# Performance work log

Measured on AMD Instinct MI355X. Metric: run time of the kernel, lower is better.

The kernel has to match this reference:

```python
import jax, jax.numpy as jnp
import numpy as np

B, T, U, D, V = 2, 512, 128, 512, 1024


def setup_inputs() -> dict:
    key = jax.random.key(0)
    k1, k2, k3 = jax.random.split(key, 3)
    encoder_outputs = jax.random.normal(k1, (B, T, D), dtype=jnp.float32)
    decoder_outputs = jax.random.normal(k2, (B, U, D), dtype=jnp.float32)
    # fc = Linear(2*D, V, bias=False): weight shape (V, 2*D)
    W = jax.random.normal(k3, (V, 2 * D), dtype=jnp.float32) * (1.0 / np.sqrt(2 * D))
    return {"encoder_outputs": encoder_outputs, "decoder_outputs": decoder_outputs, "W": W}


def reference(encoder_outputs, decoder_outputs, W):
    # Faithful to: cat(enc.repeat over U, dec.repeat over T, dim=-1) @ W.T
    # Since the Linear has no bias, splitting W into encoder/decoder halves and
    # broadcast-adding the two projections is exactly the same math, without
    # materializing the (B,T,U,2D) concat tensor.
    d = encoder_outputs.shape[-1]
    W_enc = W[:, :d]   # (V, D) acts on encoder half
    W_dec = W[:, d:]   # (V, D) acts on decoder half
    enc_proj = jnp.einsum("btd,vd->btv", encoder_outputs, W_enc)  # (B,T,V)
    dec_proj = jnp.einsum("bud,vd->buv", decoder_outputs, W_dec)  # (B,U,V)
    # (B,T,U,V)
    return enc_proj[:, :, None, :] + dec_proj[:, None, :, :]
```

## Files before the change

### kernel.cpp

```cpp
#include <hip/hip_runtime.h>

#define BB 2
#define TT 512
#define UU 128
#define DD 512
#define VV 1024

typedef float float4v __attribute__((ext_vector_type(4)));
typedef float f32x4   __attribute__((ext_vector_type(4)));
typedef short short8  __attribute__((ext_vector_type(8)));

__device__ __forceinline__ unsigned short f2bf(float f) {
    unsigned u = __builtin_bit_cast(unsigned, f);
    unsigned r = (u + 0x7FFFu + ((u >> 16) & 1u)) >> 16;
    return (unsigned short)r;
}

__device__ __forceinline__ short8 pack_bf16_8(float4v lo, float4v hi) {
    short8 r;
    r[0] = (short)f2bf(lo.x); r[1] = (short)f2bf(lo.y);
    r[2] = (short)f2bf(lo.z); r[3] = (short)f2bf(lo.w);
    r[4] = (short)f2bf(hi.x); r[5] = (short)f2bf(hi.y);
    r[6] = (short)f2bf(hi.z); r[7] = (short)f2bf(hi.w);
    return r;
}

__global__ __launch_bounds__(256) void proj_gemm_mfma(
    const float* __restrict__ Aenc,
    const float* __restrict__ Adec,
    const float* __restrict__ W,
    float* __restrict__ Cenc,
    float* __restrict__ Cdec)
{
    __shared__ alignas(16) unsigned short sA[64][40];
    __shared__ alignas(16) unsigned short sB[64][40];

    const int bid = blockIdx.x;
    const float* A; const float* Wp; float* C;
    int tile_m, tile_n;
    if (bid < 256) {
        A = Aenc; Wp = W;      C = Cenc;
        tile_m = bid >> 4; tile_n = bid & 15;
    } else {
        int b2 = bid - 256;
        A = Adec; Wp = W + DD; C = Cdec;
        tile_m = b2 >> 4; tile_n = b2 & 15;
    }
    const int row0 = tile_m * 64;
    const int col0 = tile_n * 64;

    const int tid  = threadIdx.x;
    const int lane = tid & 63;
    const int wave = tid >> 6;
    const int wr   = wave >> 1;
    const int wc   = wave & 1;
    const int lrow = lane & 15;
    const int kg   = lane >> 4;

    const int srow = tid >> 2;
    const int schk = tid & 3;

    f32x4 acc[2][2] = {};

    for (int k0 = 0; k0 < DD; k0 += 32) {
        const float* ap = &A [(size_t)(row0 + srow) * DD      + k0 + schk * 8];
        const float* wp = &Wp[(size_t)(col0 + srow) * (2*DD)  + k0 + schk * 8];
        float4v a0 = *(const float4v*)ap;
        float4v a1 = *(const float4v*)(ap + 4);
        float4v w0 = *(const float4v*)wp;
        float4v w1 = *(const float4v*)(wp + 4);
        short8 av = pack_bf16_8(a0, a1);
        short8 wv = pack_bf16_8(w0, w1);

        __syncthreads();
        *(short8*)&sA[srow][schk * 8] = av;
        *(short8*)&sB[srow][schk * 8] = wv;
        __syncthreads();

        short8 af0 = *(const short8*)&sA[wr * 32 +      lrow][kg * 8];
        short8 af1 = *(const short8*)&sA[wr * 32 + 16 + lrow][kg * 8];
        short8 bf0 = *(const short8*)&sB[wc * 32 +      lrow][kg * 8];
        short8 bf1 = *(const short8*)&sB[wc * 32 + 16 + lrow][kg * 8];

        acc[0][0] = __builtin_amdgcn_mfma_f32_16x16x32_bf16(af0, bf0, acc[0][0], 0, 0, 0);
        acc[0][1] = __builtin_amdgcn_mfma_f32_16x16x32_bf16(af0, bf1, acc[0][1], 0, 0, 0);
        acc[1][0] = __builtin_amdgcn_mfma_f32_16x16x32_bf16(af1, bf0, acc[1][0], 0, 0, 0);
        acc[1][1] = __builtin_amdgcn_mfma_f32_16x16x32_bf16(af1, bf1, acc[1][1], 0, 0, 0);
    }

    #pragma unroll
    for (int mi = 0; mi < 2; ++mi) {
        #pragma unroll
        for (int ni = 0; ni < 2; ++ni) {
            const int r0 = row0 + wr * 32 + mi * 16 + kg * 4;
            const int c  = col0 + wc * 32 + ni * 16 + lrow;
            #pragma unroll
            for (int j = 0; j < 4; ++j)
                C[(size_t)(r0 + j) * VV + c] = acc[mi][ni][j];
        }
    }
}

__global__ __launch_bounds__(256) void bcast_add_kernel(
    const float* __restrict__ enc_proj,
    const float* __restrict__ dec_proj,
    float* __restrict__ out)
{
    const int blk  = blockIdx.x;
    const int bt   = blk >> 1;
    const int half = blk & 1;
    const int b    = bt >> 9;
    const int tid  = threadIdx.x;
    const int voff = tid * 4;

    float4v e = *(const float4v*)&enc_proj[(size_t)bt * VV + voff];
    const float* dbase = dec_proj + (size_t)b * UU * VV;
    float*       obase = out      + (size_t)bt * UU * VV;

    const int u0 = half * (UU / 2);
    #pragma unroll 4
    for (int u = u0; u < u0 + (UU / 2); ++u) {
        float4v d = *(const float4v*)&dbase[(size_t)u * VV + voff];
        float4v r = e + d;
        __builtin_nontemporal_store(r, (float4v*)&obase[(size_t)u * VV + voff]);
    }
}

extern "C" void kernel_launch(void* const* d_in, const int* in_sizes, int n_in,
                              void* d_out, int out_size, void* d_ws, size_t ws_size,
                              hipStream_t stream) {
    (void)in_sizes; (void)n_in; (void)out_size; (void)ws_size;
    const float* enc = (const float*)d_in[0];
    const float* dec = (const float*)d_in[1];
    const float* W   = (const float*)d_in[2];
    float* out = (float*)d_out;

    float* enc_proj = (float*)d_ws;
    float* dec_proj = enc_proj + (size_t)BB * TT * VV;

    proj_gemm_mfma<<<dim3(320), dim3(256), 0, stream>>>(enc, dec, W, enc_proj, dec_proj);
    bcast_add_kernel<<<dim3(BB * TT * 2), dim3(256), 0, stream>>>(enc_proj, dec_proj, out);
}
```

Before: 540.7 us.

## Fuse encoder projection GEMM with broadcast-add epilogue, separate decoder GEMM

Splits the projection into a small decoder GEMM kernel and an encoder GEMM kernel whose epilogue stages the tile in shared memory and writes all U broadcast sums directly. This removes the enc_proj workspace round trip and the separate broadcast kernel. The trade-off is that the large output write is now done by only 256 blocks, one per CU, with a strided row pattern, which reduces store parallelism.

```diff
diff --git a/kernel.cpp b/kernel.cpp
--- a/kernel.cpp
+++ b/kernel.cpp
@@ -25,29 +25,19 @@
     return r;
 }
 
-__global__ __launch_bounds__(256) void proj_gemm_mfma(
-    const float* __restrict__ Aenc,
+__global__ __launch_bounds__(256) void dec_gemm_mfma(
     const float* __restrict__ Adec,
     const float* __restrict__ W,
-    float* __restrict__ Cenc,
     float* __restrict__ Cdec)
 {
     __shared__ alignas(16) unsigned short sA[64][40];
     __shared__ alignas(16) unsigned short sB[64][40];
 
-    const int bid = blockIdx.x;
-    const float* A; const float* Wp; float* C;
-    int tile_m, tile_n;
-    if (bid < 256) {
-        A = Aenc; Wp = W;      C = Cenc;
-        tile_m = bid >> 4; tile_n = bid & 15;
-    } else {
-        int b2 = bid - 256;
-        A = Adec; Wp = W + DD; C = Cdec;
-        tile_m = b2 >> 4; tile_n = b2 & 15;
-    }
+    const int tile_m = blockIdx.x >> 4;
+    const int tile_n = blockIdx.x & 15;
     const int row0 = tile_m * 64;
     const int col0 = tile_n * 64;
+    const float* Wp = W + DD;
 
     const int tid  = threadIdx.x;
     const int lane = tid & 63;
@@ -56,15 +46,14 @@
     const int wc   = wave & 1;
     const int lrow = lane & 15;
     const int kg   = lane >> 4;
-
     const int srow = tid >> 2;
     const int schk = tid & 3;
 
     f32x4 acc[2][2] = {};
 
     for (int k0 = 0; k0 < DD; k0 += 32) {
-        const float* ap = &A [(size_t)(row0 + srow) * DD      + k0 + schk * 8];
-        const float* wp = &Wp[(size_t)(col0 + srow) * (2*DD)  + k0 + schk * 8];
+        const float* ap = &Adec[(size_t)(row0 + srow) * DD     + k0 + schk * 8];
+        const float* wp = &Wp  [(size_t)(col0 + srow) * (2*DD) + k0 + schk * 8];
         float4v a0 = *(const float4v*)ap;
         float4v a1 = *(const float4v*)(ap + 4);
         float4v w0 = *(const float4v*)wp;
@@ -89,40 +78,99 @@
     }
 
     #pragma unroll
-    for (int mi = 0; mi < 2; ++mi) {
+    for (int mi = 0; mi < 2; ++mi)
         #pragma unroll
         for (int ni = 0; ni < 2; ++ni) {
             const int r0 = row0 + wr * 32 + mi * 16 + kg * 4;
             const int c  = col0 + wc * 32 + ni * 16 + lrow;
             #pragma unroll
             for (int j = 0; j < 4; ++j)
-                C[(size_t)(r0 + j) * VV + c] = acc[mi][ni][j];
+                Cdec[(size_t)(r0 + j) * VV + c] = acc[mi][ni][j];
         }
-    }
 }
 
-__global__ __launch_bounds__(256) void bcast_add_kernel(
-    const float* __restrict__ enc_proj,
+__global__ __launch_bounds__(256) void enc_gemm_bcast(
+    const float* __restrict__ Aenc,
+    const float* __restrict__ W,
     const float* __restrict__ dec_proj,
     float* __restrict__ out)
 {
-    const int blk  = blockIdx.x;
-    const int bt   = blk >> 1;
-    const int half = blk & 1;
-    const int b    = bt >> 9;
+    __shared__ alignas(16) unsigned short sA[64][40];
+    __shared__ alignas(16) unsigned short sB[64][40];
+    __shared__ alignas(16) float sT[64][68];
+
+    const int tile_m = blockIdx.x >> 4;
+    const int tile_n = blockIdx.x & 15;
+    const int row0 = tile_m * 64;
+    const int col0 = tile_n * 64;
+
     const int tid  = threadIdx.x;
-    const int voff = tid * 4;
+    const int lane = tid & 63;
+    const int wave = tid >> 6;
+    const int wr   = wave >> 1;
+    const int wc   = wave & 1;
+    const int lrow = lane & 15;
+    const int kg   = lane >> 4;
+    const int srow = tid >> 2;
+    const int schk = tid & 3;
 
-    float4v e = *(const float4v*)&enc_proj[(size_t)bt * VV + voff];
-    const float* dbase = dec_proj + (size_t)b * UU * VV;
-    float*       obase = out      + (size_t)bt * UU * VV;
+    f32x4 acc[2][2] = {};
 
-    const int u0 = half * (UU / 2);
-    #pragma unroll 4
-    for (int u = u0; u < u0 + (UU / 2); ++u) {
-        float4v d = *(const float4v*)&dbase[(size_t)u * VV + voff];
-        float4v r = e + d;
-        __builtin_nontemporal_store(r, (float4v*)&obase[(size_t)u * VV + voff]);
+    for (int k0 = 0; k0 < DD; k0 += 32) {
+        const float* ap = &Aenc[(size_t)(row0 + srow) * DD     + k0 + schk * 8];
+        const float* wp = &W   [(size_t)(col0 + srow) * (2*DD) + k0 + schk * 8];
+        float4v a0 = *(const float4v*)ap;
+        float4v a1 = *(const float4v*)(ap + 4);
+        float4v w0 = *(const float4v*)wp;
+        float4v w1 = *(const float4v*)(wp + 4);
+        short8 av = pack_bf16_8(a0, a1);
+        short8 wv = pack_bf16_8(w0, w1);
+
+        __syncthreads();
+        *(short8*)&sA[srow][schk * 8] = av;
+        *(short8*)&sB[srow][schk * 8] = wv;
+        __syncthreads();
+
+        short8 af0 = *(const short8*)&sA[wr * 32 +      lrow][kg * 8];
+        short8 af1 = *(const short8*)&sA[wr * 32 + 16 + lrow][kg * 8];
+        short8 bf0 = *(const short8*)&sB[wc * 32 +      lrow][kg * 8];
+        short8 bf1 = *(const short8*)&sB[wc * 32 + 16 + lrow][kg * 8];
+
+        acc[0][0] = __builtin_amdgcn_mfma_f32_16x16x32_bf16(af0, bf0, acc[0][0], 0, 0, 0);
+        acc[0][1] = __builtin_amdgcn_mfma_f32_16x16x32_bf16(af0, bf1, acc[0][1], 0, 0, 0);
+        acc[1][0] = __builtin_amdgcn_mfma_f32_16x16x32_bf16(af1, bf0, acc[1][0], 0, 0, 0);
+        acc[1][1] = __builtin_amdgcn_mfma_f32_16x16x32_bf16(af1, bf1, acc[1][1], 0, 0, 0);
+    }
+
+    #pragma unroll
+    for (int mi = 0; mi < 2; ++mi)
+        #pragma unroll
+        for (int ni = 0; ni < 2; ++ni) {
+            const int r0 = wr * 32 + mi * 16 + kg * 4;
+            const int c  = wc * 32 + ni * 16 + lrow;
+            #pragma unroll
+            for (int j = 0; j < 4; ++j)
+                sT[r0 + j][c] = acc[mi][ni][j];
+        }
+    __syncthreads();
+
+    const int vq = tid & 15;
+    const int pr = tid >> 4;
+    const int b  = row0 >> 9;
+
+    const float* dbase = dec_proj + ((size_t)b * UU) * VV + col0 + vq * 4;
+    float* obase = out + ((size_t)(row0 + pr) * UU) * VV + col0 + vq * 4;
+    const size_t tstep = (size_t)16 * UU * VV;
+
+    #pragma unroll 2
+    for (int u = 0; u < UU; ++u) {
+        float4v d = *(const float4v*)&dbase[(size_t)u * VV];
+        float* op = obase + (size_t)u * VV;
+        #pragma unroll
+        for (int tr = 0; tr < 4; ++tr) {
+            float4v e = *(const float4v*)&sT[tr * 16 + pr][vq * 4];
+            __builtin_nontemporal_store(e + d, (float4v*)(op + tr * tstep));
+        }
     }
 }
 
@@ -135,9 +183,8 @@
     const float* W   = (const float*)d_in[2];
     float* out = (float*)d_out;
 
-    float* enc_proj = (float*)d_ws;
-    float* dec_proj = enc_proj + (size_t)BB * TT * VV;
+    float* dec_proj = (float*)d_ws;
 
-    proj_gemm_mfma<<<dim3(320), dim3(256), 0, stream>>>(enc, dec, W, enc_proj, dec_proj);
-    bcast_add_kernel<<<dim3(BB * TT * 2), dim3(256), 0, stream>>>(enc_proj, dec_proj, out);
+    dec_gemm_mfma<<<dim3(64),  dim3(256), 0, stream>>>(dec, W, dec_proj);
+    enc_gemm_bcast<<<dim3(256), dim3(256), 0, stream>>>(enc, W, dec_proj, out);
 }
```

New measurement: 564.8 us. 1.04x slower.
